# Optimization experiments

Measured on AMD Instinct MI355X. Metric: run time of the kernel, lower is better.

The kernel has to match this reference:

```python
import jax, jax.numpy as jnp
import numpy as np

VOCAB = 100000
DIM = 128
B = 16384
O = 10  # outside window size
K = 10  # negative samples per outside word


def setup_inputs() -> dict:
    key = jax.random.key(0)
    k1, k2, k3, k4, k5 = jax.random.split(key, 5)
    center_vectors = jax.random.normal(k1, (VOCAB, DIM), dtype=jnp.float32)
    outside_vectors = jax.random.normal(k2, (VOCAB, DIM), dtype=jnp.float32)
    center_word_index = jax.random.randint(k3, (B,), 0, VOCAB, dtype=jnp.int32)
    outside_word_indices = jax.random.randint(k4, (B, O), 0, VOCAB, dtype=jnp.int32)
    negative_samples = jax.random.randint(k5, (B, O, K), 0, VOCAB, dtype=jnp.int32)
    return {
        "center_vectors": center_vectors,
        "outside_vectors": outside_vectors,
        "center_word_index": center_word_index,
        "outside_word_indices": outside_word_indices,
        "negative_samples": negative_samples,
    }


def reference(center_vectors, outside_vectors, center_word_index,
              outside_word_indices, negative_samples):
    # PAD token has index 0; masked pairs must contribute 0 to the loss.
    mask_X = outside_word_indices == 0                       # [B, O] padded outside words
    neg = jnp.where(mask_X[..., None], 0, negative_samples)  # zero negs under padded positions
    mask_W = neg == 0                                        # [B, O, K] padded negatives

    Z = center_vectors[center_word_index]                    # [B, D]
    X = outside_vectors[outside_word_indices]                # [B, O, D]
    W = outside_vectors[neg]                                 # [B, O, K, D]

    pos_score = jnp.einsum('bod,bd->bo', X, Z)               # u_o . v_c
    neg_score = jnp.einsum('bokd,bd->bok', W, Z)             # u_k . v_c

    # In torch, masked scores are set to +inf so sigmoid->1 and log->0;
    # equivalently zero out masked log-sigmoid terms.
    left = jnp.where(mask_X, 0.0, jax.nn.log_sigmoid(pos_score))          # [B, O]
    right = jnp.where(mask_W, 0.0, jax.nn.log_sigmoid(-neg_score)).sum(-1)  # [B, O]

    losses = -(left + right).sum(axis=1)                     # [B]
    return losses
```

## Files before the change

### kernel.cpp

```cpp
#include <hip/hip_runtime.h>
#include <math.h>


#define O_WIN 10
#define K_NEG 10
#define DIM   128
#define ROWS  (O_WIN * (K_NEG + 1))

__device__ __forceinline__ unsigned pack2_bf16(float a, float b) {
    unsigned ua = __float_as_uint(a);
    unsigned ub = __float_as_uint(b);
    ua = (ua + 0x7FFFu + ((ua >> 16) & 1u)) >> 16;
    ub = (ub + 0x7FFFu + ((ub >> 16) & 1u)) >> 16;
    return ua | (ub << 16);
}

__global__ __launch_bounds__(256) void convert_bf16_kernel(
    const float* __restrict__ src, unsigned* __restrict__ dst, int n8)
{
    const int i = blockIdx.x * 256 + threadIdx.x;
    if (i >= n8) return;
    const float4 a = reinterpret_cast<const float4*>(src)[2 * i];
    const float4 b = reinterpret_cast<const float4*>(src)[2 * i + 1];
    uint4 o;
    o.x = pack2_bf16(a.x, a.y);
    o.y = pack2_bf16(a.z, a.w);
    o.z = pack2_bf16(b.x, b.y);
    o.w = pack2_bf16(b.z, b.w);
    reinterpret_cast<uint4*>(dst)[i] = o;
}

__global__ __launch_bounds__(256) void w2v_neg_loss_bf16_kernel(
    const float*    __restrict__ center,
    const unsigned* __restrict__ outsideb,
    const int*      __restrict__ cidx,
    const int*      __restrict__ owi,
    const int*      __restrict__ negs,
    float*          __restrict__ out)
{
    const int tid  = threadIdx.x;
    const int wave = tid >> 6;
    const int lane = tid & 63;
    const int sub  = lane & 7;
    const int grp  = lane >> 3;

    const int b = blockIdx.x * 4 + wave;

    const int    c    = cidx[b];
    const float* zrow = center + (size_t)c * DIM;
    float zf[2][8];
    #pragma unroll
    for (int q = 0; q < 2; ++q) {
        const float4 lo = *reinterpret_cast<const float4*>(zrow + q * 64 + sub * 8);
        const float4 hi = *reinterpret_cast<const float4*>(zrow + q * 64 + sub * 8 + 4);
        zf[q][0] = lo.x; zf[q][1] = lo.y; zf[q][2] = lo.z; zf[q][3] = lo.w;
        zf[q][4] = hi.x; zf[q][5] = hi.y; zf[q][6] = hi.z; zf[q][7] = hi.w;
    }

    const int* ow_b  = owi  + (size_t)b * O_WIN;
    const int* neg_b = negs + (size_t)b * (O_WIN * K_NEG);

    float acc = 0.f;

    #pragma unroll 2
    for (int it = 0; it < 14; ++it) {
        const int  r   = grp + (it << 3);
        const bool inr = (r < ROWS);
        const int  rr  = inr ? r : 0;
        const int  o   = rr / 11;
        const int  j   = rr - o * 11;
        const int  ow  = ow_b[o];
        const int  nx  = neg_b[o * K_NEG + (j == 0 ? 0 : j - 1)];
        const int  idx = (j == 0) ? ow : nx;
        const bool valid = inr && (ow != 0) && (idx != 0);

        const uint4* wrow = reinterpret_cast<const uint4*>(
            outsideb + (size_t)idx * (DIM / 2));

        float p = 0.f;
        #pragma unroll
        for (int q = 0; q < 2; ++q) {
            const uint4 w = wrow[q * 8 + sub];
            const unsigned u[4] = { w.x, w.y, w.z, w.w };
            #pragma unroll
            for (int k = 0; k < 4; ++k) {
                const float flo = __uint_as_float(u[k] << 16);
                const float fhi = __uint_as_float(u[k] & 0xFFFF0000u);
                p += flo * zf[q][2 * k] + fhi * zf[q][2 * k + 1];
            }
        }
        p += __shfl_xor(p, 1);
        p += __shfl_xor(p, 2);
        p += __shfl_xor(p, 4);

        const float score = (j == 0) ? p : -p;
        const float ls = fminf(score, 0.f) - __logf(1.f + __expf(-fabsf(score)));
        acc += valid ? ls : 0.f;
    }

    acc += __shfl_xor(acc, 8);
    acc += __shfl_xor(acc, 16);
    acc += __shfl_xor(acc, 32);

    if (lane == 0) out[b] = -acc;
}

__global__ __launch_bounds__(256) void w2v_neg_loss_f32_kernel(
    const float* __restrict__ center,
    const float* __restrict__ outside,
    const int*   __restrict__ cidx,
    const int*   __restrict__ owi,
    const int*   __restrict__ negs,
    float*       __restrict__ out)
{
    const int tid  = threadIdx.x;
    const int wave = tid >> 6;
    const int lane = tid & 63;
    const int sub  = lane & 7;
    const int grp  = lane >> 3;
    const int b = blockIdx.x * 4 + wave;

    const int    c    = cidx[b];
    const float* zrow = center + (size_t)c * DIM;
    float4 zf[4];
    #pragma unroll
    for (int q = 0; q < 4; ++q)
        zf[q] = *reinterpret_cast<const float4*>(zrow + q * 32 + sub * 4);

    const int* ow_b  = owi  + (size_t)b * O_WIN;
    const int* neg_b = negs + (size_t)b * (O_WIN * K_NEG);
    float acc = 0.f;

    #pragma unroll 2
    for (int it = 0; it < 14; ++it) {
        const int  r   = grp + (it << 3);
        const bool inr = (r < ROWS);
        const int  rr  = inr ? r : 0;
        const int  o   = rr / 11;
        const int  j   = rr - o * 11;
        const int  ow  = ow_b[o];
        const int  nx  = neg_b[o * K_NEG + (j == 0 ? 0 : j - 1)];
        const int  idx = (j == 0) ? ow : nx;
        const bool valid = inr && (ow != 0) && (idx != 0);

        const float* wrow = outside + (size_t)idx * DIM;
        float p = 0.f;
        #pragma unroll
        for (int q = 0; q < 4; ++q) {
            const float4 w = *reinterpret_cast<const float4*>(wrow + q * 32 + sub * 4);
            p += w.x * zf[q].x + w.y * zf[q].y + w.z * zf[q].z + w.w * zf[q].w;
        }
        p += __shfl_xor(p, 1);
        p += __shfl_xor(p, 2);
        p += __shfl_xor(p, 4);

        const float score = (j == 0) ? p : -p;
        const float ls = fminf(score, 0.f) - log1pf(expf(-fabsf(score)));
        acc += valid ? ls : 0.f;
    }
    acc += __shfl_xor(acc, 8);
    acc += __shfl_xor(acc, 16);
    acc += __shfl_xor(acc, 32);
    if (lane == 0) out[b] = -acc;
}

extern "C" void kernel_launch(void* const* d_in, const int* in_sizes, int n_in,
                              void* d_out, int out_size, void* d_ws, size_t ws_size,
                              hipStream_t stream) {
    const float* center  = (const float*)d_in[0];
    const float* outside = (const float*)d_in[1];
    const int*   cw      = (const int*)d_in[2];
    const int*   ow      = (const int*)d_in[3];
    const int*   ng      = (const int*)d_in[4];
    float*       out     = (float*)d_out;

    const int B    = in_sizes[2];
    const int nOut = in_sizes[1];

    if (ws_size >= (size_t)nOut * sizeof(unsigned short)) {
        unsigned* outsideb = (unsigned*)d_ws;
        const int n8 = nOut / 8;
        convert_bf16_kernel<<<(n8 + 255) / 256, 256, 0, stream>>>(
            outside, outsideb, n8);
        w2v_neg_loss_bf16_kernel<<<B / 4, 256, 0, stream>>>(
            center, outsideb, cw, ow, ng, out);
    } else {
        w2v_neg_loss_f32_kernel<<<B / 4, 256, 0, stream>>>(
            center, outside, cw, ow, ng, out);
    }
}
```

Baseline: 178.1 us.

## Quantize outside vectors to per-row int8 and use sdot4 dot products

Replaces the bf16 conversion pass with a per-row absmax int8 quantization of the outside table, and quantizes the center vector per row too, computing the dot products with packed int8 sdot4 and rescaling. The main-kernel gather shrinks to 128 bytes per row plus a scale, and the quantize pass writes half as much as the bf16 conversion did. The loss reduction is also reworked so each lane evaluates only two log-sigmoids instead of fourteen. The trade-off is lower precision: int8 quantization of both operands may push scores past the reference tolerance.

```diff
diff --git a/kernel.cpp b/kernel.cpp
--- a/kernel.cpp
+++ b/kernel.cpp
@@ -6,33 +6,78 @@
 #define K_NEG 10
 #define DIM   128
 #define ROWS  (O_WIN * (K_NEG + 1))
-
-__device__ __forceinline__ unsigned pack2_bf16(float a, float b) {
-    unsigned ua = __float_as_uint(a);
-    unsigned ub = __float_as_uint(b);
-    ua = (ua + 0x7FFFu + ((ua >> 16) & 1u)) >> 16;
-    ub = (ub + 0x7FFFu + ((ub >> 16) & 1u)) >> 16;
-    return ua | (ub << 16);
-}
-
-__global__ __launch_bounds__(256) void convert_bf16_kernel(
-    const float* __restrict__ src, unsigned* __restrict__ dst, int n8)
+#define VROW_U32 (DIM / 4)
+
+#if defined(__has_builtin)
+#  if __has_builtin(__builtin_amdgcn_sdot4)
+#    define HAVE_SDOT4 1
+#  endif
+#endif
+
+__device__ __forceinline__ int dot4acc(unsigned a, unsigned b, int c) {
+#ifdef HAVE_SDOT4
+    return __builtin_amdgcn_sdot4((int)a, (int)b, c, false);
+#else
+    #pragma unroll
+    for (int k = 0; k < 4; ++k) {
+        const int xa = (int)(a << (24 - 8 * k)) >> 24;
+        const int xb = (int)(b << (24 - 8 * k)) >> 24;
+        c += xa * xb;
+    }
+    return c;
+#endif
+}
+
+__device__ __forceinline__ unsigned pack4_q(float4 f, float inv) {
+    const int a = (int)rintf(f.x * inv) & 0xFF;
+    const int b = (int)rintf(f.y * inv) & 0xFF;
+    const int c = (int)rintf(f.z * inv) & 0xFF;
+    const int d = (int)rintf(f.w * inv) & 0xFF;
+    return (unsigned)(a | (b << 8) | (c << 16) | (d << 24));
+}
+
+__device__ __forceinline__ float logsig(float x) {
+    return fminf(x, 0.f) - log1pf(__expf(-fabsf(x)));
+}
+
+__global__ __launch_bounds__(256) void quant_rows_kernel(
+    const float* __restrict__ src,
+    unsigned*    __restrict__ wq,
+    float*       __restrict__ wscale,
+    int vocab)
 {
-    const int i = blockIdx.x * 256 + threadIdx.x;
-    if (i >= n8) return;
-    const float4 a = reinterpret_cast<const float4*>(src)[2 * i];
-    const float4 b = reinterpret_cast<const float4*>(src)[2 * i + 1];
+    const int tid = threadIdx.x;
+    const int sub = tid & 7;
+    const int row = blockIdx.x * 32 + (tid >> 3);
+    if (row >= vocab) return;
+
+    const float* r = src + (size_t)row * DIM + sub * 16;
+    float4 f[4];
+    float m = 0.f;
+    #pragma unroll
+    for (int u = 0; u < 4; ++u) {
+        f[u] = *reinterpret_cast<const float4*>(r + u * 4);
+        m = fmaxf(m, fmaxf(fmaxf(fabsf(f[u].x), fabsf(f[u].y)),
+                           fmaxf(fabsf(f[u].z), fabsf(f[u].w))));
+    }
+    m = fmaxf(m, __shfl_xor(m, 1));
+    m = fmaxf(m, __shfl_xor(m, 2));
+    m = fmaxf(m, __shfl_xor(m, 4));
+    const float inv = (m > 0.f) ? 127.f / m : 0.f;
+
     uint4 o;
-    o.x = pack2_bf16(a.x, a.y);
-    o.y = pack2_bf16(a.z, a.w);
-    o.z = pack2_bf16(b.x, b.y);
-    o.w = pack2_bf16(b.z, b.w);
-    reinterpret_cast<uint4*>(dst)[i] = o;
-}
-
-__global__ __launch_bounds__(256) void w2v_neg_loss_bf16_kernel(
+    o.x = pack4_q(f[0], inv);
+    o.y = pack4_q(f[1], inv);
+    o.z = pack4_q(f[2], inv);
+    o.w = pack4_q(f[3], inv);
+    *reinterpret_cast<uint4*>(wq + (size_t)row * VROW_U32 + sub * 4) = o;
+    if (sub == 0) wscale[row] = m * (1.f / 127.f);
+}
+
+__global__ __launch_bounds__(256) void w2v_i8_kernel(
     const float*    __restrict__ center,
-    const unsigned* __restrict__ outsideb,
+    const unsigned* __restrict__ wq,
+    const float*    __restrict__ wscale,
     const int*      __restrict__ cidx,
     const int*      __restrict__ owi,
     const int*      __restrict__ negs,
@@ -46,23 +91,30 @@
 
     const int b = blockIdx.x * 4 + wave;
 
-    const int    c    = cidx[b];
-    const float* zrow = center + (size_t)c * DIM;
-    float zf[2][8];
-    #pragma unroll
-    for (int q = 0; q < 2; ++q) {
-        const float4 lo = *reinterpret_cast<const float4*>(zrow + q * 64 + sub * 8);
-        const float4 hi = *reinterpret_cast<const float4*>(zrow + q * 64 + sub * 8 + 4);
-        zf[q][0] = lo.x; zf[q][1] = lo.y; zf[q][2] = lo.z; zf[q][3] = lo.w;
-        zf[q][4] = hi.x; zf[q][5] = hi.y; zf[q][6] = hi.z; zf[q][7] = hi.w;
-    }
+    const float* zrow = center + (size_t)cidx[b] * DIM + sub * 16;
+    float4 zf[4];
+    float zm = 0.f;
+    #pragma unroll
+    for (int u = 0; u < 4; ++u) {
+        zf[u] = *reinterpret_cast<const float4*>(zrow + u * 4);
+        zm = fmaxf(zm, fmaxf(fmaxf(fabsf(zf[u].x), fabsf(zf[u].y)),
+                             fmaxf(fabsf(zf[u].z), fabsf(zf[u].w))));
+    }
+    zm = fmaxf(zm, __shfl_xor(zm, 1));
+    zm = fmaxf(zm, __shfl_xor(zm, 2));
+    zm = fmaxf(zm, __shfl_xor(zm, 4));
+    const float zinv = (zm > 0.f) ? 127.f / zm : 0.f;
+    const float zsc  = zm * (1.f / 127.f);
+    unsigned zq[4];
+    #pragma unroll
+    for (int u = 0; u < 4; ++u) zq[u] = pack4_q(zf[u], zinv);
 
     const int* ow_b  = owi  + (size_t)b * O_WIN;
     const int* neg_b = negs + (size_t)b * (O_WIN * K_NEG);
 
-    float acc = 0.f;
-
-    #pragma unroll 2
+    float sel0 = 1e30f, sel1 = 1e30f;
+
+    #pragma unroll
     for (int it = 0; it < 14; ++it) {
         const int  r   = grp + (it << 3);
         const bool inr = (r < ROWS);
@@ -74,30 +126,33 @@
         const int  idx = (j == 0) ? ow : nx;
         const bool valid = inr && (ow != 0) && (idx != 0);
 
-        const uint4* wrow = reinterpret_cast<const uint4*>(
-            outsideb + (size_t)idx * (DIM / 2));
-
-        float p = 0.f;
-        #pragma unroll
-        for (int q = 0; q < 2; ++q) {
-            const uint4 w = wrow[q * 8 + sub];
-            const unsigned u[4] = { w.x, w.y, w.z, w.w };
-            #pragma unroll
-            for (int k = 0; k < 4; ++k) {
-                const float flo = __uint_as_float(u[k] << 16);
-                const float fhi = __uint_as_float(u[k] & 0xFFFF0000u);
-                p += flo * zf[q][2 * k] + fhi * zf[q][2 * k + 1];
-            }
-        }
-        p += __shfl_xor(p, 1);
-        p += __shfl_xor(p, 2);
-        p += __shfl_xor(p, 4);
-
-        const float score = (j == 0) ? p : -p;
-        const float ls = fminf(score, 0.f) - __logf(1.f + __expf(-fabsf(score)));
-        acc += valid ? ls : 0.f;
-    }
-
+        const uint4 w = *reinterpret_cast<const uint4*>(
+            wq + (size_t)idx * VROW_U32 + sub * 4);
+        const float wsc = wscale[idx];
+
+        int d = 0;
+        d = dot4acc(w.x, zq[0], d);
+        d = dot4acc(w.y, zq[1], d);
+        d = dot4acc(w.z, zq[2], d);
+        d = dot4acc(w.w, zq[3], d);
+        d += __shfl_xor(d, 1);
+        d += __shfl_xor(d, 2);
+        d += __shfl_xor(d, 4);
+
+        const float p     = (float)d * (wsc * zsc);
+        float       score = (j == 0) ? p : -p;
+        score = valid ? score : 1e30f;
+
+        const bool claim = ((it & 7) == sub);
+        if (it < 8) sel0 = claim ? score : sel0;
+        else        sel1 = claim ? score : sel1;
+    }
+
+    float acc = logsig(sel0) + logsig(sel1);
+
+    acc += __shfl_xor(acc, 1);
+    acc += __shfl_xor(acc, 2);
+    acc += __shfl_xor(acc, 4);
     acc += __shfl_xor(acc, 8);
     acc += __shfl_xor(acc, 16);
     acc += __shfl_xor(acc, 32);
@@ -174,16 +229,20 @@
     const int*   ng      = (const int*)d_in[4];
     float*       out     = (float*)d_out;
 
-    const int B    = in_sizes[2];
-    const int nOut = in_sizes[1];
-
-    if (ws_size >= (size_t)nOut * sizeof(unsigned short)) {
-        unsigned* outsideb = (unsigned*)d_ws;
-        const int n8 = nOut / 8;
-        convert_bf16_kernel<<<(n8 + 255) / 256, 256, 0, stream>>>(
-            outside, outsideb, n8);
-        w2v_neg_loss_bf16_kernel<<<B / 4, 256, 0, stream>>>(
-            center, outsideb, cw, ow, ng, out);
+    const int B     = in_sizes[2];
+    const int nOut  = in_sizes[1];
+    const int vocab = nOut / DIM;
+
+    const size_t wq_bytes = (size_t)vocab * DIM;
+    const size_t need     = wq_bytes + (size_t)vocab * 4;
+
+    if (ws_size >= need) {
+        unsigned* wq     = (unsigned*)d_ws;
+        float*    wscale = (float*)((char*)d_ws + wq_bytes);
+        quant_rows_kernel<<<(vocab + 31) / 32, 256, 0, stream>>>(
+            outside, wq, wscale, vocab);
+        w2v_i8_kernel<<<B / 4, 256, 0, stream>>>(
+            center, wq, wscale, cw, ow, ng, out);
     } else {
         w2v_neg_loss_f32_kernel<<<B / 4, 256, 0, stream>>>(
             center, outside, cw, ow, ng, out);
```

Measured after the change: 148.8 us. 1.2x faster.
